# Optimization experiments

Measured on AMD Instinct MI355X. Metric: run time of the kernel, lower is better.

The kernel has to match this reference:

```python
import jax, jax.numpy as jnp
import numpy as np

B, S, D = 4, 2048, 512
H = 8
DH = D // H  # depth per head = 64
SCALE = 1.0 / np.sqrt(np.float32(D))  # NOTE: original divides by sqrt(feature_size), not sqrt(depth)
EPS = 1e-5


def setup_inputs() -> dict:
    key = jax.random.key(0)
    ks = jax.random.split(key, 10)
    std = 1.0 / np.sqrt(D)
    inp = {
        "x": jax.random.normal(ks[0], (B, S, D), dtype=jnp.float32),
        "w_q": jax.random.uniform(ks[1], (D, D), jnp.float32, -std, std),
        "b_q": jax.random.uniform(ks[2], (D,), jnp.float32, -std, std),
        "w_k": jax.random.uniform(ks[3], (D, D), jnp.float32, -std, std),
        "b_k": jax.random.uniform(ks[4], (D,), jnp.float32, -std, std),
        "w_v": jax.random.uniform(ks[5], (D, D), jnp.float32, -std, std),
        "b_v": jax.random.uniform(ks[6], (D,), jnp.float32, -std, std),
        "w_o": jax.random.uniform(ks[7], (D, D), jnp.float32, -std, std),
        "b_o": jax.random.uniform(ks[8], (D,), jnp.float32, -std, std),
        "ln_gamma": jnp.ones((D,), jnp.float32),
        "ln_beta": jnp.zeros((D,), jnp.float32),
    }
    return inp


def _split_heads(t):
    # [B, S, D] -> [B, H, S, DH]
    return t.reshape(B, S, H, DH).transpose(0, 2, 1, 3)


def reference(x, w_q, b_q, w_k, b_k, w_v, b_v, w_o, b_o, ln_gamma, ln_beta):
    q = _split_heads(x @ w_q.T + b_q)
    k = _split_heads(x @ w_k.T + b_k)
    v = _split_heads(x @ w_v.T + b_v)
    # scores: [B, H, S, S], scaled by 1/sqrt(feature_size) per the original
    scores = jnp.einsum("bhqd,bhkd->bhqk", q, k) * SCALE
    alpha = jax.nn.softmax(scores, axis=-1)
    context = jnp.einsum("bhqk,bhkd->bhqd", alpha, v)
    context = context.transpose(0, 2, 1, 3).reshape(B, S, D)
    out = context @ w_o.T + b_o
    # residual + LayerNorm
    y = out + x
    mu = jnp.mean(y, axis=-1, keepdims=True)
    var = jnp.mean(jnp.square(y - mu), axis=-1, keepdims=True)
    y = (y - mu) * jax.lax.rsqrt(var + EPS)
    return y * ln_gamma + ln_beta
```

## Files before the change

kernel.cpp:

```cpp
#include <hip/hip_runtime.h>
#include <hip/hip_bf16.h>
#include <math.h>

#define BB 4
#define SS 2048
#define DD 512
#define HH 8
#define DHH 64
#define MROWS (BB*SS)

constexpr float SCALE  = 0.044194173824159216f;
constexpr float QSCALE = (float)(0.044194173824159216 * 1.4426950408889634);
constexpr float LN_EPS = 1e-5f;

typedef __attribute__((ext_vector_type(8)))  short bf16x8;
typedef __attribute__((ext_vector_type(4)))  float f32x4;
typedef __attribute__((ext_vector_type(16))) float f32x16;

__device__ __forceinline__ ushort f2bf(float f) {
    __hip_bfloat16 h = __float2bfloat16(f);
    ushort u; __builtin_memcpy(&u, &h, 2);
    return u;
}

__device__ __forceinline__ float exp2_hw(float x) {
#if __has_builtin(__builtin_amdgcn_exp2f)
    return __builtin_amdgcn_exp2f(x);
#else
    return exp2f(x);
#endif
}

__device__ __forceinline__ unsigned cvt_pk_bf16(float lo, float hi) {
    unsigned r;
    asm("v_cvt_pk_bf16_f32 %0, %1, %2" : "=v"(r) : "v"(lo), "v"(hi));
    return r;
}
__device__ __forceinline__ void plane_swap(unsigned &a, unsigned &b) {
    asm("v_permlane32_swap_b32 %0, %1" : "+v"(a), "+v"(b));
}
__device__ __forceinline__ void plane_swapf(float &a, float &b) {
    asm("v_permlane32_swap_b32 %0, %1" : "+v"(a), "+v"(b));
}
__device__ __forceinline__ bf16x8 pack4(unsigned a0, unsigned a1, unsigned b0, unsigned b1) {
    union { unsigned u[4]; bf16x8 v; } x;
    x.u[0] = a0; x.u[1] = a1; x.u[2] = b0; x.u[3] = b1;
    return x.v;
}

__device__ __forceinline__ void gload16(const void* gsrc, void* lds_dst) {
    __builtin_amdgcn_global_load_lds(
        (const __attribute__((address_space(1))) unsigned int*)gsrc,
        (__attribute__((address_space(3))) unsigned int*)lds_dst,
        16, 0, 0);
}

__global__ __launch_bounds__(256) void cast_kernel(
    const float* __restrict__ x,
    const float* __restrict__ wq, const float* __restrict__ wk,
    const float* __restrict__ wv, const float* __restrict__ wo,
    const float* __restrict__ bq, const float* __restrict__ bk,
    const float* __restrict__ bv,
    ushort* __restrict__ xb, ushort* __restrict__ wb, float* __restrict__ biasc)
{
    const int gid = blockIdx.x * 256 + threadIdx.x;
    if (gid < 1536) {
        float v = gid < 512 ? bq[gid] * QSCALE
                : gid < 1024 ? bk[gid - 512] : bv[gid - 1024];
        biasc[gid] = v;
    }
    const int NX4 = (MROWS * DD) / 4;
    const int NW4 = (DD * DD) / 4;
    const int total = NX4 + 4 * NW4;
    for (int i = gid; i < total; i += gridDim.x * 256) {
        float4 v; ushort4 o;
        if (i < NX4) {
            v = ((const float4*)x)[i];
            o.x = f2bf(v.x); o.y = f2bf(v.y); o.z = f2bf(v.z); o.w = f2bf(v.w);
            ((ushort4*)xb)[i] = o;
        } else {
            int j = i - NX4;
            int which = j >> 16;
            int off = j & 65535;
            const float4* src = which == 0 ? (const float4*)wq
                              : which == 1 ? (const float4*)wk
                              : which == 2 ? (const float4*)wv : (const float4*)wo;
            v = src[off];
            float scl = which == 0 ? QSCALE : 1.0f;
            o.x = f2bf(v.x * scl); o.y = f2bf(v.y * scl);
            o.z = f2bf(v.z * scl); o.w = f2bf(v.w * scl);
            ((ushort4*)wb)[j] = o;
        }
    }
}

__device__ __forceinline__ void stage_tile(const ushort* __restrict__ g, int k0,
                                           ushort* lbuf, int t)
{
    #pragma unroll
    for (int i = 0; i < 4; ++i) {
        int cc = i * 256 + t;
        int row = cc >> 3, slot = cc & 7;
        gload16(g + row * DD + k0 + ((slot ^ (row & 7)) << 3), lbuf + cc * 8);
    }
}

__device__ __forceinline__ void mma_step(const ushort* Abuf, const ushort* Bbuf,
                                         int wr, int wc, int c, int g,
                                         f32x4 (&acc)[4][4])
{
    bf16x8 af[2][4], bf[2][4];
    #pragma unroll
    for (int kc = 0; kc < 2; ++kc) {
        int sw = ((kc * 4 + g) ^ (c & 7)) << 4;
        #pragma unroll
        for (int mi = 0; mi < 4; ++mi)
            af[kc][mi] = *(const bf16x8*)((const char*)Abuf + (wr*64 + mi*16 + c)*128 + sw);
        #pragma unroll
        for (int ni = 0; ni < 4; ++ni)
            bf[kc][ni] = *(const bf16x8*)((const char*)Bbuf + (wc*64 + ni*16 + c)*128 + sw);
    }
    __builtin_amdgcn_s_setprio(1);
    #pragma unroll
    for (int kc = 0; kc < 2; ++kc)
        #pragma unroll
        for (int mi = 0; mi < 4; ++mi)
            #pragma unroll
            for (int ni = 0; ni < 4; ++ni)
                acc[mi][ni] = __builtin_amdgcn_mfma_f32_16x16x32_bf16(
                    af[kc][mi], bf[kc][ni], acc[mi][ni], 0, 0, 0);
    __builtin_amdgcn_s_setprio(0);
}

__global__ __launch_bounds__(256) void qkv_mm(
    const ushort* __restrict__ xb, const ushort* __restrict__ wb,
    const float* __restrict__ biasc,
    ushort* __restrict__ Qb, ushort* __restrict__ Kb, ushort* __restrict__ Vtb)
{
    __shared__ ushort Abuf[128*64];
    __shared__ ushort Bbuf[128*64];
    const int t = threadIdx.x, w = t >> 6, lane = t & 63;
    const int wr = w >> 1, wc = w & 1, c = lane & 15, g = lane >> 4;
    const int nblk = blockIdx.x, mblk = blockIdx.y;

    const ushort* Ag = xb + (size_t)mblk * 128 * DD;
    const ushort* Bg = wb + (size_t)nblk * 128 * DD;

    f32x4 acc[4][4] = {};

    for (int k0 = 0; k0 < DD; k0 += 64) {
        stage_tile(Ag, k0, Abuf, t);
        stage_tile(Bg, k0, Bbuf, t);
        __syncthreads();
        mma_step(Abuf, Bbuf, wr, wc, c, g, acc);
        __syncthreads();
    }

    const int n0 = nblk * 128;
    const int proj = n0 >> 9;
    #pragma unroll
    for (int mi = 0; mi < 4; ++mi) {
        int m = mblk*128 + wr*64 + mi*16 + g*4;
        int bi = m >> 11, s = m & 2047;
        int tile = s >> 6, row = s & 63, sub = s & 7;
        #pragma unroll
        for (int ni = 0; ni < 4; ++ni) {
            int ng = n0 + wc*64 + ni*16 + c;
            float bias = biasc[ng];
            int col = ng & 511, h = col >> 6, d = col & 63;
            if (proj == 2) {
                size_t off = ((((size_t)(bi*HH + h)*32 + tile)*8 + (row >> 3))*512)
                           + d*8 + sub;
                ushort4 o = { f2bf(acc[mi][ni][0] + bias), f2bf(acc[mi][ni][1] + bias),
                              f2bf(acc[mi][ni][2] + bias), f2bf(acc[mi][ni][3] + bias) };
                *(ushort4*)&Vtb[off] = o;
            } else if (proj == 1) {
                size_t base = ((((size_t)(bi*HH + h)*32 + tile)*8 + (d >> 3))*512)
                            + (d & 7);
                #pragma unroll
                for (int rg = 0; rg < 4; ++rg)
                    Kb[base + (size_t)(row + rg)*8] = f2bf(acc[mi][ni][rg] + bias);
            } else {
                #pragma unroll
                for (int rg = 0; rg < 4; ++rg)
                    Qb[(((size_t)bi*HH + h)*SS + (s + rg))*DHH + d] = f2bf(acc[mi][ni][rg] + bias);
            }
        }
    }
}

__global__ __launch_bounds__(256) void oproj_mm(
    const ushort* __restrict__ ctx, const ushort* __restrict__ wob,
    const float* __restrict__ bo, const float* __restrict__ resid,
    float* __restrict__ out)
{
    __shared__ ushort Abuf[128*64];
    __shared__ ushort Bbuf[128*64];
    const int t = threadIdx.x, w = t >> 6, lane = t & 63;
    const int wr = w >> 1, wc = w & 1, c = lane & 15, g = lane >> 4;
    const int nblk = blockIdx.x, mblk = blockIdx.y;

    const ushort* Ag = ctx + (size_t)mblk * 128 * DD;
    const ushort* Bg = wob + (size_t)nblk * 128 * DD;

    f32x4 acc[4][4] = {};

    for (int k0 = 0; k0 < DD; k0 += 64) {
        stage_tile(Ag, k0, Abuf, t);
        stage_tile(Bg, k0, Bbuf, t);
        __syncthreads();
        mma_step(Abuf, Bbuf, wr, wc, c, g, acc);
        __syncthreads();
    }

    #pragma unroll
    for (int mi = 0; mi < 4; ++mi) {
        int m = mblk*128 + wr*64 + mi*16 + g*4;
        #pragma unroll
        for (int ni = 0; ni < 4; ++ni) {
            int ng = nblk*128 + wc*64 + ni*16 + c;
            float bias = bo[ng];
            #pragma unroll
            for (int rg = 0; rg < 4; ++rg) {
                int mm = m + rg;
                out[(size_t)mm*DD + ng] = acc[mi][ni][rg] + bias + resid[(size_t)mm*DD + ng];
            }
        }
    }
}

__global__ __launch_bounds__(512) void attn_kernel(
    const ushort* __restrict__ Q, const ushort* __restrict__ K,
    const ushort* __restrict__ Vt, ushort* __restrict__ ctx)
{
    __shared__ ushort Ks[2][2][64*64];
    __shared__ ushort Vts[2][2][64*64];

    const int t = threadIdx.x;
    const int w = t >> 6, l = t & 63;
    const int ln31 = l & 31, hi = l >> 5;
    const int qb = w & 3, kvh = w >> 2;

    const int id  = blockIdx.x;
    const int swz = (id & 7) * 64 + (id >> 3);
    const int qt = swz & 15;
    const int h  = (swz >> 4) & 7;
    const int b  = swz >> 7;
    const size_t bh = (size_t)b * HH + h;
    const int q0 = qt*128 + qb*32;

    const ushort* Qp = Q + (bh * SS + (size_t)q0 + ln31) * DHH;
    bf16x8 qf[4];
    #pragma unroll
    for (int s = 0; s < 4; ++s)
        qf[s] = *(const bf16x8*)&Qp[s*16 + hi*8];

    const int t2 = t & 255;
    const int NT = SS/64/2;

#define ATTN_STAGE(kvi, bi_) do {                                          \
        const size_t tb_ = (bh*32 + (size_t)(kvh*NT + (kvi))) << 12;       \
        const ushort* kp_ = K  + tb_;                                      \
        const ushort* vp_ = Vt + tb_;                                      \
        gload16(kp_ + t2*8,         &Ks[kvh][bi_][t2*8]);                  \
        gload16(kp_ + (t2+256)*8,   &Ks[kvh][bi_][(t2+256)*8]);            \
        gload16(vp_ + t2*8,         &Vts[kvh][bi_][t2*8]);                 \
        gload16(vp_ + (t2+256)*8,   &Vts[kvh][bi_][(t2+256)*8]);           \
    } while (0)

    f32x16 ot[2] = {};
    float lsum = 0.f;

    ATTN_STAGE(0, 0);

    for (int kv = 0; kv < NT; ++kv) {
        const int cur = kv & 1;
        __syncthreads();
        if (kv + 1 < NT) ATTN_STAGE(kv + 1, cur ^ 1);

        const ushort* Kc = Ks[kvh][cur];
        const ushort* Vc = Vts[kvh][cur];

        f32x16 st[2];
        __builtin_amdgcn_s_setprio(1);
        #pragma unroll
        for (int kt = 0; kt < 2; ++kt) {
            f32x16 z = {};
            #pragma unroll
            for (int s = 0; s < 4; ++s) {
                bf16x8 kf = *(const bf16x8*)((const char*)Kc
                            + ((2*s + hi) << 10) + ((kt*32 + ln31) << 4));
                z = __builtin_amdgcn_mfma_f32_32x32x16_bf16(kf, qf[s], z, 0, 0, 0);
            }
            st[kt] = z;
        }
        __builtin_amdgcn_s_setprio(0);

        #pragma unroll
        for (int kt = 0; kt < 2; ++kt)
            #pragma unroll
            for (int i = 0; i < 16; ++i)
                st[kt][i] = exp2_hw(st[kt][i]);

        {
            float ps[16];
            #pragma unroll
            for (int i = 0; i < 16; ++i) ps[i] = st[0][i] + st[1][i];
            #pragma unroll
            for (int i = 0; i < 8; ++i)  ps[i] += ps[i+8];
            #pragma unroll
            for (int i = 0; i < 4; ++i)  ps[i] += ps[i+4];
            float psum = (ps[0] + ps[1]) + (ps[2] + ps[3]);
            float pa = psum, pb2 = psum;
            plane_swapf(pa, pb2);
            lsum += pa + pb2;
        }

        unsigned dk[2][4][2];
        #pragma unroll
        for (int kt = 0; kt < 2; ++kt)
            #pragma unroll
            for (int rb = 0; rb < 4; ++rb) {
                dk[kt][rb][0] = cvt_pk_bf16(st[kt][4*rb+0], st[kt][4*rb+1]);
                dk[kt][rb][1] = cvt_pk_bf16(st[kt][4*rb+2], st[kt][4*rb+3]);
            }
        bf16x8 pb[2][2];
        #pragma unroll
        for (int kt = 0; kt < 2; ++kt)
            #pragma unroll
            for (int s2 = 0; s2 < 2; ++s2) {
                unsigned a0 = dk[kt][2*s2][0], b0 = dk[kt][2*s2+1][0];
                unsigned a1 = dk[kt][2*s2][1], b1 = dk[kt][2*s2+1][1];
                plane_swap(a0, b0);
                plane_swap(a1, b1);
                pb[kt][s2] = pack4(a0, a1, b0, b1);
            }

        __builtin_amdgcn_s_setprio(1);
        #pragma unroll
        for (int kt = 0; kt < 2; ++kt)
            #pragma unroll
            for (int s2 = 0; s2 < 2; ++s2)
                #pragma unroll
                for (int dt = 0; dt < 2; ++dt) {
                    bf16x8 vf = *(const bf16x8*)((const char*)Vc
                                + ((kt*4 + 2*s2 + hi) << 10) + ((dt*32 + ln31) << 4));
                    ot[dt] = __builtin_amdgcn_mfma_f32_32x32x16_bf16(vf, pb[kt][s2], ot[dt], 0, 0, 0);
                }
        __builtin_amdgcn_s_setprio(0);
    }
#undef ATTN_STAGE

    __syncthreads();
    float* comb = (float*)&Ks[0][0][0];
    float* p = comb + (size_t)(qb*64 + l) * 33;
    if (kvh == 0) {
        #pragma unroll
        for (int i = 0; i < 16; ++i) { p[i] = ot[0][i]; p[16+i] = ot[1][i]; }
        p[32] = lsum;
    }
    __syncthreads();
    if (kvh == 1) {
        const float rl = 1.f / (lsum + p[32]);
        ushort* outp = ctx + ((size_t)b*SS + q0 + ln31) * DD + h*DHH;
        #pragma unroll
        for (int dt = 0; dt < 2; ++dt)
            #pragma unroll
            for (int rb = 0; rb < 4; ++rb) {
                ushort4 o = { f2bf((ot[dt][4*rb+0] + p[dt*16+4*rb+0])*rl),
                              f2bf((ot[dt][4*rb+1] + p[dt*16+4*rb+1])*rl),
                              f2bf((ot[dt][4*rb+2] + p[dt*16+4*rb+2])*rl),
                              f2bf((ot[dt][4*rb+3] + p[dt*16+4*rb+3])*rl) };
                *(ushort4*)&outp[dt*32 + rb*8 + hi*4] = o;
            }
    }
}

__global__ __launch_bounds__(256) void ln_kernel(
    const float* __restrict__ y, const float* __restrict__ gamma,
    const float* __restrict__ beta, float* __restrict__ out)
{
    const int row = blockIdx.x;
    const int t = threadIdx.x;
    const float* yr = y + (size_t)row * DD;

    float2 v = *(const float2*)&yr[t*2];
    float s  = v.x + v.y;
    float sq = v.x*v.x + v.y*v.y;
    #pragma unroll
    for (int off = 1; off < 64; off <<= 1) {
        s  += __shfl_xor(s,  off);
        sq += __shfl_xor(sq, off);
    }
    __shared__ float ss[4], ssq[4];
    int wv = t >> 6;
    if ((t & 63) == 0) { ss[wv] = s; ssq[wv] = sq; }
    __syncthreads();
    s  = ss[0] + ss[1] + ss[2] + ss[3];
    sq = ssq[0] + ssq[1] + ssq[2] + ssq[3];

    float mean = s * (1.0f / DD);
    float var  = sq * (1.0f / DD) - mean * mean;
    float rstd = rsqrtf(var + LN_EPS);

    float2 g  = *(const float2*)&gamma[t*2];
    float2 be = *(const float2*)&beta[t*2];
    float2 o;
    o.x = (v.x - mean) * rstd * g.x + be.x;
    o.y = (v.y - mean) * rstd * g.y + be.y;
    *(float2*)&out[(size_t)row * DD + t*2] = o;
}

extern "C" void kernel_launch(void* const* d_in, const int* in_sizes, int n_in,
                              void* d_out, int out_size, void* d_ws, size_t ws_size,
                              hipStream_t stream)
{
    const float* x     = (const float*)d_in[0];
    const float* wq    = (const float*)d_in[1];
    const float* bq    = (const float*)d_in[2];
    const float* wk    = (const float*)d_in[3];
    const float* bk    = (const float*)d_in[4];
    const float* wv    = (const float*)d_in[5];
    const float* bv    = (const float*)d_in[6];
    const float* wo    = (const float*)d_in[7];
    const float* bo    = (const float*)d_in[8];
    const float* gamma = (const float*)d_in[9];
    const float* beta  = (const float*)d_in[10];

    char* wsb = (char*)d_ws;
    const size_t MB = 1u << 20;
    ushort* xb    = (ushort*)(wsb + 0*MB);
    ushort* wb    = (ushort*)(wsb + 8*MB);
    float*  biasc = (float* )(wsb + 10*MB);
    ushort* Qb    = (ushort*)(wsb + 11*MB);
    ushort* Kb    = (ushort*)(wsb + 19*MB);
    ushort* Vtb   = (ushort*)(wsb + 27*MB);
    ushort* ctxb  = (ushort*)(wsb + 35*MB);
    float*  ybuf  = (float*)(wsb + 11*MB);

    cast_kernel<<<2048, 256, 0, stream>>>(x, wq, wk, wv, wo, bq, bk, bv,
                                          xb, wb, biasc);
    {
        dim3 grid(12, 64);
        qkv_mm<<<grid, 256, 0, stream>>>(xb, wb, biasc, Qb, Kb, Vtb);
    }
    {
        attn_kernel<<<512, 512, 0, stream>>>(Qb, Kb, Vtb, ctxb);
    }
    {
        dim3 grid(4, 64);
        oproj_mm<<<grid, 256, 0, stream>>>(ctxb, wb + 3*DD*DD, bo, x, ybuf);
    }
    ln_kernel<<<MROWS, 256, 0, stream>>>(ybuf, gamma, beta, (float*)d_out);
}
```

Baseline: 104.1 us.

## Software-pipeline attention PV with QK^T and stage QKV epilogue through LDS

The attention loop is restructured so the P·V MFMAs for the previous KV tile are issued after the QK^T MFMAs of the current tile, with softmax/pack deferred. V gets a triple buffer in LDS to support the one-tile lag. The aim is to overlap exp/pack VALU work with matrix work. Separately, the QKV projection epilogue now transposes each wave's tile through LDS and writes Q, K and Vt with coalesced 16-byte stores. Q moves to a tiled layout so the attention kernel's Q loads are contiguous. Launch bounds add an occupancy hint of 4, which may pressure registers given the extra live P fragments.

```diff
diff --git a/kernel.cpp b/kernel.cpp
--- a/kernel.cpp
+++ b/kernel.cpp
@@ -137,8 +137,10 @@
     const float* __restrict__ biasc,
     ushort* __restrict__ Qb, ushort* __restrict__ Kb, ushort* __restrict__ Vtb)
 {
-    __shared__ ushort Abuf[128*64];
-    __shared__ ushort Bbuf[128*64];
+    __shared__ char smem[34816];
+    ushort* Abuf = (ushort*)smem;
+    ushort* Bbuf = (ushort*)(smem + 16384);
+
     const int t = threadIdx.x, w = t >> 6, lane = t & 63;
     const int wr = w >> 1, wc = w & 1, c = lane & 15, g = lane >> 4;
     const int nblk = blockIdx.x, mblk = blockIdx.y;
@@ -156,35 +158,63 @@
         __syncthreads();
     }
 
-    const int n0 = nblk * 128;
-    const int proj = n0 >> 9;
-    #pragma unroll
-    for (int mi = 0; mi < 4; ++mi) {
-        int m = mblk*128 + wr*64 + mi*16 + g*4;
-        int bi = m >> 11, s = m & 2047;
-        int tile = s >> 6, row = s & 63, sub = s & 7;
-        #pragma unroll
-        for (int ni = 0; ni < 4; ++ni) {
-            int ng = n0 + wc*64 + ni*16 + c;
-            float bias = biasc[ng];
-            int col = ng & 511, h = col >> 6, d = col & 63;
-            if (proj == 2) {
-                size_t off = ((((size_t)(bi*HH + h)*32 + tile)*8 + (row >> 3))*512)
-                           + d*8 + sub;
-                ushort4 o = { f2bf(acc[mi][ni][0] + bias), f2bf(acc[mi][ni][1] + bias),
-                              f2bf(acc[mi][ni][2] + bias), f2bf(acc[mi][ni][3] + bias) };
-                *(ushort4*)&Vtb[off] = o;
-            } else if (proj == 1) {
-                size_t base = ((((size_t)(bi*HH + h)*32 + tile)*8 + (d >> 3))*512)
-                            + (d & 7);
+    ushort* E = (ushort*)(smem + (size_t)w * 8704);
+    const int n0w  = nblk*128 + wc*64;
+    const int proj = n0w >> 9;
+    const int h    = (n0w & 511) >> 6;
+    const int m0w  = mblk*128 + wr*64;
+    const int bi   = m0w >> 11;
+    const int st0  = m0w & 2047;
+
+    if (proj == 2) {
+        #pragma unroll
+        for (int mi = 0; mi < 4; ++mi)
+            #pragma unroll
+            for (int ni = 0; ni < 4; ++ni) {
+                float bias = biasc[n0w + ni*16 + c];
+                ushort4 pk = { f2bf(acc[mi][ni][0]+bias), f2bf(acc[mi][ni][1]+bias),
+                               f2bf(acc[mi][ni][2]+bias), f2bf(acc[mi][ni][3]+bias) };
+                *(ushort4*)&E[(ni*16 + c)*68 + mi*16 + g*4] = pk;
+            }
+    } else {
+        #pragma unroll
+        for (int mi = 0; mi < 4; ++mi)
+            #pragma unroll
+            for (int ni = 0; ni < 4; ++ni) {
+                float bias = biasc[n0w + ni*16 + c];
                 #pragma unroll
                 for (int rg = 0; rg < 4; ++rg)
-                    Kb[base + (size_t)(row + rg)*8] = f2bf(acc[mi][ni][rg] + bias);
-            } else {
-                #pragma unroll
-                for (int rg = 0; rg < 4; ++rg)
-                    Qb[(((size_t)bi*HH + h)*SS + (s + rg))*DHH + d] = f2bf(acc[mi][ni][rg] + bias);
+                    E[(mi*16 + g*4 + rg)*68 + ni*16 + c] = f2bf(acc[mi][ni][rg]+bias);
             }
+    }
+
+    const int l = lane;
+    if (proj == 0) {
+        char* base = (char*)Qb + ((size_t)(bi*HH + h)*64 + (st0 >> 5) + (l >> 5)) * 4096;
+        #pragma unroll
+        for (int j = 0; j < 8; ++j) {
+            uint2 v0 = *(uint2*)&E[l*68 + j*8];
+            uint2 v1 = *(uint2*)&E[l*68 + j*8 + 4];
+            uint4 v = { v0.x, v0.y, v1.x, v1.y };
+            *(uint4*)(base + j*512 + (l & 31)*16) = v;
+        }
+    } else if (proj == 1) {
+        char* base = (char*)Kb + ((size_t)(bi*HH + h)*32 + (st0 >> 6)) * 8192;
+        #pragma unroll
+        for (int j = 0; j < 8; ++j) {
+            uint2 v0 = *(uint2*)&E[l*68 + j*8];
+            uint2 v1 = *(uint2*)&E[l*68 + j*8 + 4];
+            uint4 v = { v0.x, v0.y, v1.x, v1.y };
+            *(uint4*)(base + j*1024 + l*16) = v;
+        }
+    } else {
+        char* base = (char*)Vtb + ((size_t)(bi*HH + h)*32 + (st0 >> 6)) * 8192;
+        #pragma unroll
+        for (int j = 0; j < 8; ++j) {
+            uint2 v0 = *(uint2*)&E[l*68 + j*8];
+            uint2 v1 = *(uint2*)&E[l*68 + j*8 + 4];
+            uint4 v = { v0.x, v0.y, v1.x, v1.y };
+            *(uint4*)(base + j*1024 + l*16) = v;
         }
     }
 }
@@ -229,12 +259,12 @@
     }
 }
 
-__global__ __launch_bounds__(512) void attn_kernel(
+__global__ __launch_bounds__(512, 4) void attn_kernel(
     const ushort* __restrict__ Q, const ushort* __restrict__ K,
     const ushort* __restrict__ Vt, ushort* __restrict__ ctx)
 {
     __shared__ ushort Ks[2][2][64*64];
-    __shared__ ushort Vts[2][2][64*64];
+    __shared__ ushort Vts[2][3][64*64];
 
     const int t = threadIdx.x;
     const int w = t >> 6, l = t & 63;
@@ -249,106 +279,131 @@
     const size_t bh = (size_t)b * HH + h;
     const int q0 = qt*128 + qb*32;
 
-    const ushort* Qp = Q + (bh * SS + (size_t)q0 + ln31) * DHH;
+    const char* Qp = (const char*)Q + (bh*64 + (size_t)(qt*4 + qb)) * 4096;
     bf16x8 qf[4];
     #pragma unroll
     for (int s = 0; s < 4; ++s)
-        qf[s] = *(const bf16x8*)&Qp[s*16 + hi*8];
+        qf[s] = *(const bf16x8*)(Qp + (2*s + hi)*512 + ln31*16);
 
     const int t2 = t & 255;
-    const int NT = SS/64/2;
-
-#define ATTN_STAGE(kvi, bi_) do {                                          \
-        const size_t tb_ = (bh*32 + (size_t)(kvh*NT + (kvi))) << 12;       \
-        const ushort* kp_ = K  + tb_;                                      \
-        const ushort* vp_ = Vt + tb_;                                      \
-        gload16(kp_ + t2*8,         &Ks[kvh][bi_][t2*8]);                  \
-        gload16(kp_ + (t2+256)*8,   &Ks[kvh][bi_][(t2+256)*8]);            \
-        gload16(vp_ + t2*8,         &Vts[kvh][bi_][t2*8]);                 \
-        gload16(vp_ + (t2+256)*8,   &Vts[kvh][bi_][(t2+256)*8]);           \
+    const int NT = 16;
+    const size_t kvbase = bh * 32;
+
+#define ATTN_STAGE(kvi, kb_, vb_) do {                                      \
+        const size_t tb_ = (kvbase + (size_t)(kvh*NT + (kvi))) * 8192;      \
+        const char* kp_ = (const char*)K  + tb_;                            \
+        const char* vp_ = (const char*)Vt + tb_;                            \
+        gload16(kp_ + t2*16,        (char*)&Ks[kvh][kb_][0] + t2*16);       \
+        gload16(kp_ + 4096 + t2*16, (char*)&Ks[kvh][kb_][0] + 4096 + t2*16);\
+        gload16(vp_ + t2*16,        (char*)&Vts[kvh][vb_][0] + t2*16);      \
+        gload16(vp_ + 4096 + t2*16, (char*)&Vts[kvh][vb_][0] + 4096 + t2*16);\
+    } while (0)
+
+#define QKT(kb_, ST) do {                                                   \
+        const char* Kc_ = (const char*)&Ks[kvh][kb_][0];                    \
+        __builtin_amdgcn_s_setprio(1);                                      \
+        _Pragma("unroll")                                                   \
+        for (int kt = 0; kt < 2; ++kt) {                                    \
+            f32x16 z_ = {};                                                 \
+            _Pragma("unroll")                                               \
+            for (int s = 0; s < 4; ++s) {                                   \
+                bf16x8 kf_ = *(const bf16x8*)(Kc_ + ((2*s + hi) << 10)      \
+                                                  + ((kt*32 + ln31) << 4)); \
+                z_ = __builtin_amdgcn_mfma_f32_32x32x16_bf16(kf_, qf[s], z_, 0, 0, 0); \
+            }                                                               \
+            ST[kt] = z_;                                                    \
+        }                                                                   \
+        __builtin_amdgcn_s_setprio(0);                                      \
+    } while (0)
+
+#define PVSTEP(vb_, PB) do {                                                \
+        const char* Vc_ = (const char*)&Vts[kvh][vb_][0];                   \
+        __builtin_amdgcn_s_setprio(1);                                      \
+        _Pragma("unroll")                                                   \
+        for (int kt = 0; kt < 2; ++kt)                                      \
+            _Pragma("unroll")                                               \
+            for (int s2 = 0; s2 < 2; ++s2)                                  \
+                _Pragma("unroll")                                           \
+                for (int dt = 0; dt < 2; ++dt) {                            \
+                    bf16x8 vf_ = *(const bf16x8*)(Vc_ + ((kt*4 + 2*s2 + hi) << 10) \
+                                                      + ((dt*32 + ln31) << 4));    \
+                    ot[dt] = __builtin_amdgcn_mfma_f32_32x32x16_bf16(vf_, PB[kt][s2], ot[dt], 0, 0, 0); \
+                }                                                           \
+        __builtin_amdgcn_s_setprio(0);                                      \
+    } while (0)
+
+#define SOFTPACK(ST, PB) do {                                               \
+        _Pragma("unroll")                                                   \
+        for (int kt = 0; kt < 2; ++kt)                                      \
+            _Pragma("unroll")                                               \
+            for (int i = 0; i < 16; ++i)                                    \
+                ST[kt][i] = exp2_hw(ST[kt][i]);                             \
+        {                                                                   \
+            float ps_[16];                                                  \
+            _Pragma("unroll")                                               \
+            for (int i = 0; i < 16; ++i) ps_[i] = ST[0][i] + ST[1][i];      \
+            _Pragma("unroll")                                               \
+            for (int i = 0; i < 8; ++i)  ps_[i] += ps_[i+8];                \
+            _Pragma("unroll")                                               \
+            for (int i = 0; i < 4; ++i)  ps_[i] += ps_[i+4];                \
+            float psum_ = (ps_[0] + ps_[1]) + (ps_[2] + ps_[3]);            \
+            float pa_ = psum_, pb2_ = psum_;                                \
+            plane_swapf(pa_, pb2_);                                         \
+            lsum += pa_ + pb2_;                                             \
+        }                                                                   \
+        unsigned dk_[2][4][2];                                              \
+        _Pragma("unroll")                                                   \
+        for (int kt = 0; kt < 2; ++kt)                                      \
+            _Pragma("unroll")                                               \
+            for (int rb = 0; rb < 4; ++rb) {                                \
+                dk_[kt][rb][0] = cvt_pk_bf16(ST[kt][4*rb+0], ST[kt][4*rb+1]);\
+                dk_[kt][rb][1] = cvt_pk_bf16(ST[kt][4*rb+2], ST[kt][4*rb+3]);\
+            }                                                               \
+        _Pragma("unroll")                                                   \
+        for (int kt = 0; kt < 2; ++kt)                                      \
+            _Pragma("unroll")                                               \
+            for (int s2 = 0; s2 < 2; ++s2) {                                \
+                unsigned a0_ = dk_[kt][2*s2][0], b0_ = dk_[kt][2*s2+1][0];  \
+                unsigned a1_ = dk_[kt][2*s2][1], b1_ = dk_[kt][2*s2+1][1];  \
+                plane_swap(a0_, b0_);                                       \
+                plane_swap(a1_, b1_);                                       \
+                PB[kt][s2] = pack4(a0_, a1_, b0_, b1_);                     \
+            }                                                               \
+    } while (0)
+
+#define ITER(kv, PBP, PBC) do {                                             \
+        __syncthreads();                                                    \
+        if ((kv) + 1 < NT) ATTN_STAGE((kv)+1, ((kv)+1)&1, ((kv)+1)%3);      \
+        f32x16 stl[2];                                                      \
+        QKT((kv)&1, stl);                                                   \
+        PVSTEP(((kv)-1)%3, PBP);                                            \
+        SOFTPACK(stl, PBC);                                                 \
     } while (0)
 
     f32x16 ot[2] = {};
     float lsum = 0.f;
-
-    ATTN_STAGE(0, 0);
-
-    for (int kv = 0; kv < NT; ++kv) {
-        const int cur = kv & 1;
-        __syncthreads();
-        if (kv + 1 < NT) ATTN_STAGE(kv + 1, cur ^ 1);
-
-        const ushort* Kc = Ks[kvh][cur];
-        const ushort* Vc = Vts[kvh][cur];
-
-        f32x16 st[2];
-        __builtin_amdgcn_s_setprio(1);
-        #pragma unroll
-        for (int kt = 0; kt < 2; ++kt) {
-            f32x16 z = {};
-            #pragma unroll
-            for (int s = 0; s < 4; ++s) {
-                bf16x8 kf = *(const bf16x8*)((const char*)Kc
-                            + ((2*s + hi) << 10) + ((kt*32 + ln31) << 4));
-                z = __builtin_amdgcn_mfma_f32_32x32x16_bf16(kf, qf[s], z, 0, 0, 0);
-            }
-            st[kt] = z;
-        }
-        __builtin_amdgcn_s_setprio(0);
-
-        #pragma unroll
-        for (int kt = 0; kt < 2; ++kt)
-            #pragma unroll
-            for (int i = 0; i < 16; ++i)
-                st[kt][i] = exp2_hw(st[kt][i]);
-
-        {
-            float ps[16];
-            #pragma unroll
-            for (int i = 0; i < 16; ++i) ps[i] = st[0][i] + st[1][i];
-            #pragma unroll
-            for (int i = 0; i < 8; ++i)  ps[i] += ps[i+8];
-            #pragma unroll
-            for (int i = 0; i < 4; ++i)  ps[i] += ps[i+4];
-            float psum = (ps[0] + ps[1]) + (ps[2] + ps[3]);
-            float pa = psum, pb2 = psum;
-            plane_swapf(pa, pb2);
-            lsum += pa + pb2;
-        }
-
-        unsigned dk[2][4][2];
-        #pragma unroll
-        for (int kt = 0; kt < 2; ++kt)
-            #pragma unroll
-            for (int rb = 0; rb < 4; ++rb) {
-                dk[kt][rb][0] = cvt_pk_bf16(st[kt][4*rb+0], st[kt][4*rb+1]);
-                dk[kt][rb][1] = cvt_pk_bf16(st[kt][4*rb+2], st[kt][4*rb+3]);
-            }
-        bf16x8 pb[2][2];
-        #pragma unroll
-        for (int kt = 0; kt < 2; ++kt)
-            #pragma unroll
-            for (int s2 = 0; s2 < 2; ++s2) {
-                unsigned a0 = dk[kt][2*s2][0], b0 = dk[kt][2*s2+1][0];
-                unsigned a1 = dk[kt][2*s2][1], b1 = dk[kt][2*s2+1][1];
-                plane_swap(a0, b0);
-                plane_swap(a1, b1);
-                pb[kt][s2] = pack4(a0, a1, b0, b1);
-            }
-
-        __builtin_amdgcn_s_setprio(1);
-        #pragma unroll
-        for (int kt = 0; kt < 2; ++kt)
-            #pragma unroll
-            for (int s2 = 0; s2 < 2; ++s2)
-                #pragma unroll
-                for (int dt = 0; dt < 2; ++dt) {
-                    bf16x8 vf = *(const bf16x8*)((const char*)Vc
-                                + ((kt*4 + 2*s2 + hi) << 10) + ((dt*32 + ln31) << 4));
-                    ot[dt] = __builtin_amdgcn_mfma_f32_32x32x16_bf16(vf, pb[kt][s2], ot[dt], 0, 0, 0);
-                }
-        __builtin_amdgcn_s_setprio(0);
-    }
+    bf16x8 pbA[2][2], pbB[2][2];
+
+    ATTN_STAGE(0, 0, 0);
+    __syncthreads();
+    ATTN_STAGE(1, 1, 1);
+    {
+        f32x16 stl[2];
+        QKT(0, stl);
+        SOFTPACK(stl, pbA);
+    }
+
+    for (int kv = 1; kv <= 13; kv += 2) {
+        ITER(kv,     pbA, pbB);
+        ITER(kv + 1, pbB, pbA);
+    }
+    ITER(15, pbA, pbB);
+    PVSTEP(15 % 3, pbB);
+
+#undef ITER
+#undef SOFTPACK
+#undef PVSTEP
+#undef QKT
 #undef ATTN_STAGE
 
     __syncthreads();
```

Result: faster. 99.93 us (-4.0%).
